# Performance work log

Hardware: AMD Instinct MI355X
Metric: run time of the kernel (lower is better)

## Reference

```python
import jax, jax.numpy as jnp
import numpy as np
import math

NEG = -1e9  # matches torch masked_fill value -1000000000.0


def setup_inputs() -> dict:
    key = jax.random.key(0)
    k1, k2, k3, k4, k5 = jax.random.split(key, 5)
    N, M, Dk = 32, 2048, 64
    query = jax.random.normal(k1, (N, M, Dk), dtype=jnp.float32)
    key_t = jax.random.normal(k2, (N, M, Dk), dtype=jnp.float32)
    value = jax.random.normal(k3, (N, M, Dk), dtype=jnp.float32)
    key_padding_mask = jax.random.randint(k4, (N, M), 0, 2).astype(bool)
    attn_mask = jax.random.randint(k5, (M, M), 0, 2).astype(bool)
    return {
        "query": query,
        "key": key_t,
        "value": value,
        "key_padding_mask": key_padding_mask,
        "attn_mask": attn_mask,
    }


def reference(query, key, value, key_padding_mask, attn_mask):
    d = query.shape[-1]
    # scores: (N, m, n)
    scores = jnp.einsum("nmd,nkd->nmk", query, key) / math.sqrt(d)
    # key_padding_mask: (N, n) -> broadcast over query dim m
    scores = scores + jnp.where(key_padding_mask, NEG, 0.0)[:, None, :]
    # attn_mask: (m, n) -> broadcast over batch N
    scores = scores + jnp.where(attn_mask, NEG, 0.0)[None, :, :]
    attn_weights = jax.nn.softmax(scores, axis=-1)
    out = jnp.einsum("nmk,nkd->nmd", attn_weights, value)  # dropout p=0.0 is identity
    return out, attn_weights
```

## Files before the change

kernel.cpp:

```cpp
#include <hip/hip_runtime.h>
#include <stdint.h>

typedef __attribute__((ext_vector_type(8))) short v8s;
typedef __attribute__((ext_vector_type(4))) float v4f;

#define NBATCH 32
#define SEQ 2048
#define DHEAD 64

__device__ __forceinline__ unsigned short f2bf(float f) {
  unsigned int x = __float_as_uint(f);
  x += 0x7fffu + ((x >> 16) & 1u);
  return (unsigned short)(x >> 16);
}

__device__ __forceinline__ float bf2f(short s) {
  return __uint_as_float(((unsigned int)(unsigned short)s) << 16);
}

__global__ void cvt_bf16_k(const float* __restrict__ src,
                           unsigned short* __restrict__ dst, int n4) {
  int i = blockIdx.x * blockDim.x + threadIdx.x;
  if (i >= n4) return;
  float4 v = ((const float4*)src)[i];
  ushort4 o;
  o.x = f2bf(v.x); o.y = f2bf(v.y); o.z = f2bf(v.z); o.w = f2bf(v.w);
  ((ushort4*)dst)[i] = o;
}

__global__ void vtrans_k(const float* __restrict__ V,
                         unsigned short* __restrict__ Vt) {
  __shared__ float tile[64][65];
  int n = blockIdx.y, k0 = blockIdx.x * 64;
  int t = threadIdx.x;
  int c = t & 63, rb = t >> 6;
#pragma unroll
  for (int it = 0; it < 16; ++it) {
    int r = it * 4 + rb;
    tile[r][c] = V[((size_t)(n * SEQ + k0 + r)) * DHEAD + c];
  }
  __syncthreads();
#pragma unroll
  for (int it = 0; it < 16; ++it) {
    int d = it * 4 + rb;
    Vt[((size_t)(n * DHEAD + d)) * SEQ + k0 + c] = f2bf(tile[c][d]);
  }
}

__global__ void pack_am_k(const int* __restrict__ am, unsigned int* __restrict__ amT2) {
  int tid = blockIdx.x * blockDim.x + threadIdx.x;
  int k = tid & (SEQ - 1), w = tid >> 11;
  unsigned int bits = 0;
#pragma unroll 4
  for (int i = 0; i < 32; ++i)
    bits |= (am[(size_t)(w * 32 + i) * SEQ + k] != 0 ? 1u : 0u) << i;
  amT2[w * SEQ + k] = bits;
}

__global__ void pack_kpm_k(const int* __restrict__ kpm, unsigned int* __restrict__ kpmB) {
  int tid = blockIdx.x * blockDim.x + threadIdx.x;
  if (tid >= NBATCH * 64) return;
  int n = tid >> 6, w = tid & 63;
  unsigned int bits = 0;
#pragma unroll 4
  for (int i = 0; i < 32; ++i)
    bits |= (kpm[n * SEQ + w * 32 + i] != 0 ? 1u : 0u) << i;
  kpmB[n * 64 + w] = bits;
}

__global__ __launch_bounds__(512, 2)
void attn_main_k(const unsigned short* __restrict__ Qb,
                 const unsigned short* __restrict__ Kb,
                 const unsigned short* __restrict__ Vt,
                 const unsigned int* __restrict__ amT2,
                 const unsigned int* __restrict__ kpmB,
                 float* __restrict__ outO, float* __restrict__ outW) {
  __shared__ __align__(16) char smem[65536];

  const int n = blockIdx.y;
  const int row0 = blockIdx.x * 16;
  const int tid = threadIdx.x;
  const int wave = tid >> 6, lane = tid & 63;
  const int quad = lane >> 4, lq = lane & 15;
  const int colw = wave * 256;

  const unsigned short* qp = Qb + ((size_t)(n * SEQ + row0 + lq)) * DHEAD + quad * 8;
  v8s a0 = *(const v8s*)qp;
  v8s a1 = *(const v8s*)(qp + 32);

  float p[64];
  float rsum[4] = {0.f, 0.f, 0.f, 0.f};
  const int amsh = row0 & 31;
  const int amw = row0 >> 5;

#pragma unroll
  for (int kt = 0; kt < 16; ++kt) {
    const int col = colw + kt * 16 + lq;
    const unsigned short* kp = Kb + ((size_t)(n * SEQ + col)) * DHEAD + quad * 8;
    v8s b0 = *(const v8s*)kp;
    v8s b1 = *(const v8s*)(kp + 32);
    v4f c = {0.f, 0.f, 0.f, 0.f};
    c = __builtin_amdgcn_mfma_f32_16x16x32_bf16(a0, b0, c, 0, 0, 0);
    c = __builtin_amdgcn_mfma_f32_16x16x32_bf16(a1, b1, c, 0, 0, 0);
    unsigned int abits = amT2[amw * SEQ + col] >> amsh;
    unsigned int kw = kpmB[n * 64 + (colw >> 5) + (kt >> 1)];
    unsigned int kbit = (kw >> ((kt & 1) * 16 + lq)) & 1u;
#pragma unroll
    for (int r = 0; r < 4; ++r) {
      unsigned int msk = kbit | ((abits >> (quad * 4 + r)) & 1u);
      float e = msk ? 0.f : __expf(c[r] * 0.125f);
      p[kt * 4 + r] = e;
      rsum[r] += e;
    }
  }

#pragma unroll
  for (int r = 0; r < 4; ++r) {
    float s = rsum[r];
    s += __shfl_xor(s, 1);
    s += __shfl_xor(s, 2);
    s += __shfl_xor(s, 4);
    s += __shfl_xor(s, 8);
    rsum[r] = s;
  }
  float* wsum = (float*)smem;
  if (lq == 0) {
#pragma unroll
    for (int r = 0; r < 4; ++r) wsum[wave * 16 + quad * 4 + r] = rsum[r];
  }
  __syncthreads();
  float rinv[4];
#pragma unroll
  for (int r = 0; r < 4; ++r) {
    float s = 0.f;
#pragma unroll
    for (int w = 0; w < 8; ++w) s += wsum[w * 16 + quad * 4 + r];
    rinv[r] = 1.0f / s;
  }
  __syncthreads();

#pragma unroll
  for (int kt = 0; kt < 16; ++kt) {
    const int colL = colw + kt * 16 + lq;
#pragma unroll
    for (int r = 0; r < 4; ++r) {
      const int rr = quad * 4 + r;
      float pn = p[kt * 4 + r] * rinv[r];
      *(unsigned short*)(smem + rr * 4096 +
                         ((((colL >> 3) ^ (rr & 7)) << 4) | ((colL & 7) << 1))) = f2bf(pn);
    }
  }
  __syncthreads();

  v4f acc[4] = {{0.f,0.f,0.f,0.f},{0.f,0.f,0.f,0.f},{0.f,0.f,0.f,0.f},{0.f,0.f,0.f,0.f}};
#pragma unroll
  for (int ch = 0; ch < 8; ++ch) {
    const int cb = colw + ch * 32;
    v8s ap = *(const v8s*)(smem + lq * 4096 + (((((cb >> 3) + quad) ^ (lq & 7)) << 4)));
#pragma unroll
    for (int dt = 0; dt < 4; ++dt) {
      const unsigned short* vp =
          Vt + ((size_t)(n * DHEAD + dt * 16 + lq)) * SEQ + cb + quad * 8;
      v8s bp = *(const v8s*)vp;
      acc[dt] = __builtin_amdgcn_mfma_f32_16x16x32_bf16(ap, bp, acc[dt], 0, 0, 0);
    }
  }

  {
    float* wbase = outW + ((size_t)(n * SEQ + row0)) * SEQ;
#pragma unroll
    for (int ps = 0; ps < 8; ++ps) {
      const int row = wave * 2 + (ps & 1);
      const int cb8 = lane + ((ps >> 1) << 6);
      v8s pv = *(const v8s*)(smem + row * 4096 + ((cb8 ^ (row & 7)) << 4));
      float4 f0, f1;
      f0.x = bf2f(pv[0]); f0.y = bf2f(pv[1]); f0.z = bf2f(pv[2]); f0.w = bf2f(pv[3]);
      f1.x = bf2f(pv[4]); f1.y = bf2f(pv[5]); f1.z = bf2f(pv[6]); f1.w = bf2f(pv[7]);
      float* dst = wbase + (size_t)row * SEQ + (cb8 << 3);
      ((float4*)dst)[0] = f0;
      ((float4*)dst)[1] = f1;
    }
  }
  __syncthreads();

  float* olds = (float*)smem;
#pragma unroll
  for (int dt = 0; dt < 4; ++dt)
#pragma unroll
    for (int r = 0; r < 4; ++r)
      olds[wave * 1088 + (quad * 4 + r) * 68 + dt * 16 + lq] = acc[dt][r];
  __syncthreads();
#pragma unroll
  for (int s = 0; s < 2; ++s) {
    int e = tid + s * 512;
    int row = e >> 6, d = e & 63;
    float a = 0.f;
#pragma unroll
    for (int w = 0; w < 8; ++w) a += olds[w * 1088 + row * 68 + d];
    outO[((size_t)(n * SEQ + row0 + row)) * DHEAD + d] = a;
  }
}

extern "C" void kernel_launch(void* const* d_in, const int* in_sizes, int n_in,
                              void* d_out, int out_size, void* d_ws, size_t ws_size,
                              hipStream_t stream) {
  const float* Q = (const float*)d_in[0];
  const float* K = (const float*)d_in[1];
  const float* V = (const float*)d_in[2];
  const int* kpm = (const int*)d_in[3];
  const int* am = (const int*)d_in[4];

  float* outO = (float*)d_out;
  float* outW = outO + (size_t)NBATCH * SEQ * DHEAD;

  char* ws = (char*)d_ws;
  unsigned short* Qb = (unsigned short*)ws;
  unsigned short* Kb = (unsigned short*)(ws + (8u << 20));
  unsigned short* Vt = (unsigned short*)(ws + (16u << 20));
  unsigned int* amT2 = (unsigned int*)(ws + (24u << 20));
  unsigned int* kpmB = (unsigned int*)(ws + (24u << 20) + (1u << 19));

  const int n4 = NBATCH * SEQ * DHEAD / 4;
  cvt_bf16_k<<<n4 / 256, 256, 0, stream>>>(Q, Qb, n4);
  cvt_bf16_k<<<n4 / 256, 256, 0, stream>>>(K, Kb, n4);
  vtrans_k<<<dim3(SEQ / 64, NBATCH), 256, 0, stream>>>(V, Vt);
  pack_am_k<<<(SEQ * 64) / 256, 256, 0, stream>>>(am, amT2);
  pack_kpm_k<<<8, 256, 0, stream>>>(kpm, kpmB);
  attn_main_k<<<dim3(SEQ / 16, NBATCH), 512, 0, stream>>>(Qb, Kb, Vt, amT2, kpmB,
                                                          outO, outW);
}
```

Before: 814.7 us.

## Double waves per block and defer softmax normalization to drop register P buffer

The main attention kernel now runs 16 waves per block, each covering 128 key columns instead of 256. Unnormalized exponentials go straight to LDS as bf16 rather than being held in a 64-float register array, which cuts register pressure. The row normalization is applied when the attention weights are written and when the final output is reduced. The attention-weight store also moves ahead of the P·V MFMA loop so it can overlap with it. In exchange, the LDS footprint grows, the cross-wave reductions span more waves, and bf16 rounding now happens before normalization instead of after.

New measurement: 860.6 us. 5.6% more time.

```diff
diff --git a/kernel.cpp b/kernel.cpp
--- a/kernel.cpp
+++ b/kernel.cpp
@@ -68,33 +68,32 @@
   kpmB[n * 64 + w] = bits;
 }
 
-__global__ __launch_bounds__(512, 2)
+__global__ __launch_bounds__(1024, 8)
 void attn_main_k(const unsigned short* __restrict__ Qb,
                  const unsigned short* __restrict__ Kb,
                  const unsigned short* __restrict__ Vt,
                  const unsigned int* __restrict__ amT2,
                  const unsigned int* __restrict__ kpmB,
                  float* __restrict__ outO, float* __restrict__ outW) {
-  __shared__ __align__(16) char smem[65536];
+  __shared__ __align__(16) char smem[69760];
 
   const int n = blockIdx.y;
   const int row0 = blockIdx.x * 16;
   const int tid = threadIdx.x;
   const int wave = tid >> 6, lane = tid & 63;
   const int quad = lane >> 4, lq = lane & 15;
-  const int colw = wave * 256;
+  const int colw = wave * 128;
 
   const unsigned short* qp = Qb + ((size_t)(n * SEQ + row0 + lq)) * DHEAD + quad * 8;
   v8s a0 = *(const v8s*)qp;
   v8s a1 = *(const v8s*)(qp + 32);
 
-  float p[64];
   float rsum[4] = {0.f, 0.f, 0.f, 0.f};
   const int amsh = row0 & 31;
   const int amw = row0 >> 5;
 
 #pragma unroll
-  for (int kt = 0; kt < 16; ++kt) {
+  for (int kt = 0; kt < 8; ++kt) {
     const int col = colw + kt * 16 + lq;
     const unsigned short* kp = Kb + ((size_t)(n * SEQ + col)) * DHEAD + quad * 8;
     v8s b0 = *(const v8s*)kp;
@@ -107,10 +106,12 @@
     unsigned int kbit = (kw >> ((kt & 1) * 16 + lq)) & 1u;
 #pragma unroll
     for (int r = 0; r < 4; ++r) {
-      unsigned int msk = kbit | ((abits >> (quad * 4 + r)) & 1u);
+      const int rr = quad * 4 + r;
+      unsigned int msk = kbit | ((abits >> rr) & 1u);
       float e = msk ? 0.f : __expf(c[r] * 0.125f);
-      p[kt * 4 + r] = e;
       rsum[r] += e;
+      *(unsigned short*)(smem + rr * 4096 +
+                         ((((col >> 3) ^ (rr & 7)) << 4) | ((col & 7) << 1))) = f2bf(e);
     }
   }
 
@@ -123,38 +124,44 @@
     s += __shfl_xor(s, 8);
     rsum[r] = s;
   }
-  float* wsum = (float*)smem;
+  float* wsum = (float*)(smem + 65536);
   if (lq == 0) {
 #pragma unroll
     for (int r = 0; r < 4; ++r) wsum[wave * 16 + quad * 4 + r] = rsum[r];
   }
   __syncthreads();
-  float rinv[4];
-#pragma unroll
-  for (int r = 0; r < 4; ++r) {
+
+  float* totF = (float*)(smem + 69632);
+  if (tid < 16) {
     float s = 0.f;
 #pragma unroll
-    for (int w = 0; w < 8; ++w) s += wsum[w * 16 + quad * 4 + r];
-    rinv[r] = 1.0f / s;
-  }
-  __syncthreads();
-
-#pragma unroll
-  for (int kt = 0; kt < 16; ++kt) {
-    const int colL = colw + kt * 16 + lq;
-#pragma unroll
-    for (int r = 0; r < 4; ++r) {
-      const int rr = quad * 4 + r;
-      float pn = p[kt * 4 + r] * rinv[r];
-      *(unsigned short*)(smem + rr * 4096 +
-                         ((((colL >> 3) ^ (rr & 7)) << 4) | ((colL & 7) << 1))) = f2bf(pn);
+    for (int w = 0; w < 16; ++w) s += wsum[w * 16 + tid];
+    totF[tid] = s;
+  }
+  __syncthreads();
+
+  {
+    const int row = wave;
+    const float rw = 1.0f / totF[row];
+    float* dstrow = outW + ((size_t)(n * SEQ + row0 + row)) * SEQ;
+#pragma unroll
+    for (int ps = 0; ps < 4; ++ps) {
+      const int cb8 = lane + (ps << 6);
+      v8s pv = *(const v8s*)(smem + row * 4096 + ((cb8 ^ (row & 7)) << 4));
+      float4 f0, f1;
+      f0.x = bf2f(pv[0]) * rw; f0.y = bf2f(pv[1]) * rw;
+      f0.z = bf2f(pv[2]) * rw; f0.w = bf2f(pv[3]) * rw;
+      f1.x = bf2f(pv[4]) * rw; f1.y = bf2f(pv[5]) * rw;
+      f1.z = bf2f(pv[6]) * rw; f1.w = bf2f(pv[7]) * rw;
+      float* dst = dstrow + (cb8 << 3);
+      ((float4*)dst)[0] = f0;
+      ((float4*)dst)[1] = f1;
     }
   }
-  __syncthreads();
 
   v4f acc[4] = {{0.f,0.f,0.f,0.f},{0.f,0.f,0.f,0.f},{0.f,0.f,0.f,0.f},{0.f,0.f,0.f,0.f}};
 #pragma unroll
-  for (int ch = 0; ch < 8; ++ch) {
+  for (int ch = 0; ch < 4; ++ch) {
     const int cb = colw + ch * 32;
     v8s ap = *(const v8s*)(smem + lq * 4096 + (((((cb >> 3) + quad) ^ (lq & 7)) << 4)));
 #pragma unroll
@@ -165,22 +172,6 @@
       acc[dt] = __builtin_amdgcn_mfma_f32_16x16x32_bf16(ap, bp, acc[dt], 0, 0, 0);
     }
   }
-
-  {
-    float* wbase = outW + ((size_t)(n * SEQ + row0)) * SEQ;
-#pragma unroll
-    for (int ps = 0; ps < 8; ++ps) {
-      const int row = wave * 2 + (ps & 1);
-      const int cb8 = lane + ((ps >> 1) << 6);
-      v8s pv = *(const v8s*)(smem + row * 4096 + ((cb8 ^ (row & 7)) << 4));
-      float4 f0, f1;
-      f0.x = bf2f(pv[0]); f0.y = bf2f(pv[1]); f0.z = bf2f(pv[2]); f0.w = bf2f(pv[3]);
-      f1.x = bf2f(pv[4]); f1.y = bf2f(pv[5]); f1.z = bf2f(pv[6]); f1.w = bf2f(pv[7]);
-      float* dst = wbase + (size_t)row * SEQ + (cb8 << 3);
-      ((float4*)dst)[0] = f0;
-      ((float4*)dst)[1] = f1;
-    }
-  }
   __syncthreads();
 
   float* olds = (float*)smem;
@@ -190,14 +181,13 @@
     for (int r = 0; r < 4; ++r)
       olds[wave * 1088 + (quad * 4 + r) * 68 + dt * 16 + lq] = acc[dt][r];
   __syncthreads();
-#pragma unroll
-  for (int s = 0; s < 2; ++s) {
-    int e = tid + s * 512;
-    int row = e >> 6, d = e & 63;
-    float a = 0.f;
-#pragma unroll
-    for (int w = 0; w < 8; ++w) a += olds[w * 1088 + row * 68 + d];
-    outO[((size_t)(n * SEQ + row0 + row)) * DHEAD + d] = a;
+  {
+    const int row = tid >> 6, d = tid & 63;
+    float s = 0.f;
+#pragma unroll
+    for (int w = 0; w < 16; ++w) s += olds[w * 1088 + row * 68 + d];
+    s *= 1.0f / totF[row];
+    outO[((size_t)(n * SEQ + row0 + row)) * DHEAD + d] = s;
   }
 }
 
@@ -226,6 +216,6 @@
   vtrans_k<<<dim3(SEQ / 64, NBATCH), 256, 0, stream>>>(V, Vt);
   pack_am_k<<<(SEQ * 64) / 256, 256, 0, stream>>>(am, amT2);
   pack_kpm_k<<<8, 256, 0, stream>>>(kpm, kpmB);
-  attn_main_k<<<dim3(SEQ / 16, NBATCH), 512, 0, stream>>>(Qb, Kb, Vt, amT2, kpmB,
-                                                          outO, outW);
-}
+  attn_main_k<<<dim3(SEQ / 16, NBATCH), 1024, 0, stream>>>(Qb, Kb, Vt, amT2, kpmB,
+                                                           outO, outW);
+}
```
